# Kernel optimization log

Measured on AMD Instinct MI355X. Metric: run time of the kernel, lower is better.

The kernel has to match this reference:

```python
import jax, jax.numpy as jnp
import numpy as np

DIM = 4          # number of trunk networks (x, y, z, t)
H = 256          # hidden width for trunk and branch MLPs
R = 64           # CP rank
FD = 1           # field_dim
NF = 64          # Fourier feature half-width (B has shape (1, 64))
BRANCH_DIM = 256
DEPTH = 3        # MLP depth (3 hidden layers per eqx.nn.MLP semantics)


def _lin_init(key, out_dim, in_dim):
    return jax.random.normal(key, (out_dim, in_dim), dtype=jnp.float32) / jnp.sqrt(jnp.float32(in_dim))


def setup_inputs() -> dict:
    key = jax.random.key(0)
    ks = jax.random.split(key, 40)
    inp = {}
    # coordinate arrays, one per trunk: (N_i, 1)
    inp['x1'] = jax.random.uniform(ks[0], (64, 1), dtype=jnp.float32)
    inp['x2'] = jax.random.uniform(ks[1], (64, 1), dtype=jnp.float32)
    inp['x3'] = jax.random.uniform(ks[2], (64, 1), dtype=jnp.float32)
    inp['x4'] = jax.random.uniform(ks[3], (32, 1), dtype=jnp.float32)
    # branch input: batch of power maps, (B, branch_dim)
    inp['f'] = jax.random.normal(ks[4], (8, BRANCH_DIM), dtype=jnp.float32)
    # Fourier feature matrix B ~ 2*pi*N(0,1), shape (1, 64)
    inp['B'] = 2.0 * jnp.pi * jax.random.normal(ks[5], (1, NF), dtype=jnp.float32)
    # trunk ensemble params, stacked over the DIM trunks (all share shapes)
    inp['tW0'] = jnp.stack([_lin_init(ks[6 + i], H, 2 * NF) for i in range(DIM)])
    inp['tb0'] = jnp.zeros((DIM, H), dtype=jnp.float32)
    inp['tW1'] = jnp.stack([_lin_init(ks[10 + i], H, H) for i in range(DIM)])
    inp['tb1'] = jnp.zeros((DIM, H), dtype=jnp.float32)
    inp['tW2'] = jnp.stack([_lin_init(ks[14 + i], H, H) for i in range(DIM)])
    inp['tb2'] = jnp.zeros((DIM, H), dtype=jnp.float32)
    inp['tW3'] = jnp.stack([_lin_init(ks[18 + i], R * FD, H) for i in range(DIM)])
    inp['tb3'] = jnp.zeros((DIM, R * FD), dtype=jnp.float32)
    # branch MLP params
    inp['bW0'] = _lin_init(ks[30], H, BRANCH_DIM)
    inp['bb0'] = jnp.zeros((H,), dtype=jnp.float32)
    inp['bW1'] = _lin_init(ks[31], H, H)
    inp['bb1'] = jnp.zeros((H,), dtype=jnp.float32)
    inp['bW2'] = _lin_init(ks[32], H, H)
    inp['bb2'] = jnp.zeros((H,), dtype=jnp.float32)
    inp['bW3'] = _lin_init(ks[33], R * FD, H)
    inp['bb3'] = jnp.zeros((R * FD,), dtype=jnp.float32)
    return inp


def _forward(x1, x2, x3, x4, f, B,
             tW0, tb0, tW1, tb1, tW2, tb2, tW3, tb3,
             bW0, bb0, bW1, bb1, bW2, bb2, bW3, bb3):
    xs = [x1, x2, x3, x4]
    ts = []
    for i in range(DIM):
        p = xs[i] @ B                                  # (N_i, NF)
        feat = jnp.concatenate([jnp.cos(p), jnp.sin(p)], axis=1)  # (N_i, 2*NF)
        h = jax.nn.swish(feat @ tW0[i].T + tb0[i])
        h = jax.nn.swish(h @ tW1[i].T + tb1[i])
        h = jax.nn.swish(h @ tW2[i].T + tb2[i])
        t = (h @ tW3[i].T + tb3[i]).reshape(-1, FD, R)  # (N_i, y, z)
        ts.append(t)
    h = jax.nn.swish(f @ bW0.T + bb0)
    h = jax.nn.swish(h @ bW1.T + bb1)
    h = jax.nn.swish(h @ bW2.T + bb2)
    b = (h @ bW3.T + bb3).reshape(-1, FD, R)            # (B, y, z)
    # rank-R CP outer-product reconstruction: sum over z, shared field dim y
    return jnp.einsum('iyz,jyz,kyz,lyz,byz->bijkly',
                      ts[0], ts[1], ts[2], ts[3], b, optimize='optimal')


def reference(x1, x2, x3, x4, f, B,
              tW0, tb0, tW1, tb1, tW2, tb2, tW3, tb3,
              bW0, bb0, bW1, bb1, bW2, bb2, bW3, bb3):
    return _forward(x1, x2, x3, x4, f, B,
                    tW0, tb0, tW1, tb1, tW2, tb2, tW3, tb3,
                    bW0, bb0, bW1, bb1, bW2, bb2, bW3, bb3)
```

## Files before the change

### kernel.cpp

```cpp
#include <hip/hip_runtime.h>
#include <math.h>


#define HID 256
#define NFF 64

__global__ __launch_bounds__(256) void net_eval(
    const float* __restrict__ x1, const float* __restrict__ x2,
    const float* __restrict__ x3, const float* __restrict__ x4,
    const float* __restrict__ f,  const float* __restrict__ Bm,
    const float* __restrict__ tW0, const float* __restrict__ tb0,
    const float* __restrict__ tW1, const float* __restrict__ tb1,
    const float* __restrict__ tW2, const float* __restrict__ tb2,
    const float* __restrict__ tW3, const float* __restrict__ tb3,
    const float* __restrict__ bW0, const float* __restrict__ bb0,
    const float* __restrict__ bW1, const float* __restrict__ bb1,
    const float* __restrict__ bW2, const float* __restrict__ bb2,
    const float* __restrict__ bW3, const float* __restrict__ bb3,
    float* __restrict__ ws)
{
    __shared__ float bufA[HID];
    __shared__ float bufB[HID];
    const int t = threadIdx.x;
    const int bid = blockIdx.x;

    int net, row;
    if (bid < 192)      { net = bid >> 6; row = bid & 63; }
    else if (bid < 224) { net = 3;        row = bid - 192; }
    else                { net = 4;        row = bid - 224; }

    const float *W0, *B0v, *W1, *B1v, *W2, *B2v, *W3, *B3v;
    int in0;
    if (net < 4) {
        W0 = tW0 + (size_t)net * HID * 2 * NFF; B0v = tb0 + net * HID;
        W1 = tW1 + (size_t)net * HID * HID;     B1v = tb1 + net * HID;
        W2 = tW2 + (size_t)net * HID * HID;     B2v = tb2 + net * HID;
        W3 = tW3 + (size_t)net * 64 * HID;      B3v = tb3 + net * 64;
        in0 = 2 * NFF;
        const float* xp = (net == 0) ? x1 : (net == 1) ? x2 : (net == 2) ? x3 : x4;
        float xv = xp[row];
        if (t < 128) {
            float p = xv * Bm[t & 63];
            bufA[t] = (t < 64) ? cosf(p) : sinf(p);
        }
    } else {
        W0 = bW0; B0v = bb0; W1 = bW1; B1v = bb1;
        W2 = bW2; B2v = bb2; W3 = bW3; B3v = bb3;
        in0 = 256;
        bufA[t] = f[(size_t)row * 256 + t];
    }
    __syncthreads();

    {
        float acc = B0v[t];
        const float4* wr = (const float4*)(W0 + (size_t)t * in0);
        const float4* iv = (const float4*)bufA;
        const int n4 = in0 >> 2;
        for (int k = 0; k < n4; ++k) {
            float4 w = wr[k]; float4 v = iv[k];
            acc += w.x * v.x + w.y * v.y + w.z * v.z + w.w * v.w;
        }
        bufB[t] = acc / (1.0f + expf(-acc));
    }
    __syncthreads();

    {
        float acc = B1v[t];
        const float4* wr = (const float4*)(W1 + (size_t)t * HID);
        const float4* iv = (const float4*)bufB;
        for (int k = 0; k < HID / 4; ++k) {
            float4 w = wr[k]; float4 v = iv[k];
            acc += w.x * v.x + w.y * v.y + w.z * v.z + w.w * v.w;
        }
        bufA[t] = acc / (1.0f + expf(-acc));
    }
    __syncthreads();

    {
        float acc = B2v[t];
        const float4* wr = (const float4*)(W2 + (size_t)t * HID);
        const float4* iv = (const float4*)bufA;
        for (int k = 0; k < HID / 4; ++k) {
            float4 w = wr[k]; float4 v = iv[k];
            acc += w.x * v.x + w.y * v.y + w.z * v.z + w.w * v.w;
        }
        bufB[t] = acc / (1.0f + expf(-acc));
    }
    __syncthreads();

    if (t < 64) {
        float acc = B3v[t];
        const float4* wr = (const float4*)(W3 + (size_t)t * HID);
        const float4* iv = (const float4*)bufB;
        for (int k = 0; k < HID / 4; ++k) {
            float4 w = wr[k]; float4 v = iv[k];
            acc += w.x * v.x + w.y * v.y + w.z * v.z + w.w * v.w;
        }
        int base, stride;
        if      (net == 0) { base = 0;     stride = 64; }
        else if (net == 1) { base = 4096;  stride = 64; }
        else if (net == 2) { base = 8192;  stride = 64; }
        else if (net == 3) { base = 12288; stride = 32; }
        else               { base = 14336; stride = 8;  }
        ws[base + t * stride + row] = acc;
    }
}

__global__ __launch_bounds__(256) void cp_recon(
    const float* __restrict__ ws, float* __restrict__ out)
{
    __shared__ float t2s[64 * 64];
    __shared__ float t3s[64 * 32];
    __shared__ float sS[4 * 64];

    const int t = threadIdx.x;
    const int bid = blockIdx.x;
    const int b  = bid >> 10;
    const int i  = (bid >> 4) & 63;
    const int j0 = (bid & 15) * 4;

    #pragma unroll
    for (int m = 0; m < 16; ++m) {
        int g = t + m * 256;
        t2s[g] = ws[8192 + g];
    }
    #pragma unroll
    for (int m = 0; m < 8; ++m) {
        int g = t + m * 256;
        t3s[g] = ws[12288 + g];
    }
    {
        int jj = t >> 6;
        int z  = t & 63;
        sS[t] = ws[z * 64 + i] * ws[4096 + z * 64 + j0 + jj] * ws[14336 + z * 8 + b];
    }
    __syncthreads();

    const int jj   = t >> 6;
    const int lane = t & 63;
    const int k0   = (lane >> 3) * 8;
    const int l0   = (lane & 7) * 4;
    const float* sp = &sS[jj * 64];

    float4 acc[8];
    #pragma unroll
    for (int kk = 0; kk < 8; ++kk) acc[kk] = make_float4(0.f, 0.f, 0.f, 0.f);

    #pragma unroll 4
    for (int z = 0; z < 64; ++z) {
        float sz = sp[z];
        float4 t3v = *(const float4*)&t3s[z * 32 + l0];
        float4 a0  = *(const float4*)&t2s[z * 64 + k0];
        float4 a1  = *(const float4*)&t2s[z * 64 + k0 + 4];
        float4 u;
        u.x = sz * t3v.x; u.y = sz * t3v.y; u.z = sz * t3v.z; u.w = sz * t3v.w;
        float ks0 = a0.x, ks1 = a0.y, ks2 = a0.z, ks3 = a0.w;
        float ks4 = a1.x, ks5 = a1.y, ks6 = a1.z, ks7 = a1.w;
        acc[0].x += ks0 * u.x; acc[0].y += ks0 * u.y; acc[0].z += ks0 * u.z; acc[0].w += ks0 * u.w;
        acc[1].x += ks1 * u.x; acc[1].y += ks1 * u.y; acc[1].z += ks1 * u.z; acc[1].w += ks1 * u.w;
        acc[2].x += ks2 * u.x; acc[2].y += ks2 * u.y; acc[2].z += ks2 * u.z; acc[2].w += ks2 * u.w;
        acc[3].x += ks3 * u.x; acc[3].y += ks3 * u.y; acc[3].z += ks3 * u.z; acc[3].w += ks3 * u.w;
        acc[4].x += ks4 * u.x; acc[4].y += ks4 * u.y; acc[4].z += ks4 * u.z; acc[4].w += ks4 * u.w;
        acc[5].x += ks5 * u.x; acc[5].y += ks5 * u.y; acc[5].z += ks5 * u.z; acc[5].w += ks5 * u.w;
        acc[6].x += ks6 * u.x; acc[6].y += ks6 * u.y; acc[6].z += ks6 * u.z; acc[6].w += ks6 * u.w;
        acc[7].x += ks7 * u.x; acc[7].y += ks7 * u.y; acc[7].z += ks7 * u.z; acc[7].w += ks7 * u.w;
    }

    size_t base = ((size_t)((b * 64 + i) * 64 + (j0 + jj))) * 2048;
    float* op = out + base;
    #pragma unroll
    for (int kk = 0; kk < 8; ++kk) {
        *(float4*)&op[(k0 + kk) * 32 + l0] = acc[kk];
    }
}

extern "C" void kernel_launch(void* const* d_in, const int* in_sizes, int n_in,
                              void* d_out, int out_size, void* d_ws, size_t ws_size,
                              hipStream_t stream) {
    const float* x1  = (const float*)d_in[0];
    const float* x2  = (const float*)d_in[1];
    const float* x3  = (const float*)d_in[2];
    const float* x4  = (const float*)d_in[3];
    const float* f   = (const float*)d_in[4];
    const float* Bm  = (const float*)d_in[5];
    const float* tW0 = (const float*)d_in[6];
    const float* tb0 = (const float*)d_in[7];
    const float* tW1 = (const float*)d_in[8];
    const float* tb1 = (const float*)d_in[9];
    const float* tW2 = (const float*)d_in[10];
    const float* tb2 = (const float*)d_in[11];
    const float* tW3 = (const float*)d_in[12];
    const float* tb3 = (const float*)d_in[13];
    const float* bW0 = (const float*)d_in[14];
    const float* bb0 = (const float*)d_in[15];
    const float* bW1 = (const float*)d_in[16];
    const float* bb1 = (const float*)d_in[17];
    const float* bW2 = (const float*)d_in[18];
    const float* bb2 = (const float*)d_in[19];
    const float* bW3 = (const float*)d_in[20];
    const float* bb3 = (const float*)d_in[21];

    float* ws  = (float*)d_ws;
    float* out = (float*)d_out;

    hipLaunchKernelGGL(net_eval, dim3(232), dim3(256), 0, stream,
                       x1, x2, x3, x4, f, Bm,
                       tW0, tb0, tW1, tb1, tW2, tb2, tW3, tb3,
                       bW0, bb0, bW1, bb1, bW2, bb2, bW3, bb3, ws);
    hipLaunchKernelGGL(cp_recon, dim3(8192), dim3(256), 0, stream, ws, out);
}
```

Measured before the change: 399.9 us.

## Recast CP reconstruction as bf16 MFMA GEMM and warp-reduce MLP layers

```diff
diff --git a/kernel.cpp b/kernel.cpp
--- a/kernel.cpp
+++ b/kernel.cpp
@@ -2,8 +2,51 @@
 #include <math.h>
 
 
-#define HID 256
-#define NFF 64
+typedef float float4v __attribute__((ext_vector_type(4)));
+typedef short short8 __attribute__((ext_vector_type(8)));
+
+__device__ inline unsigned short f2bf(float f) {
+    union { float f; unsigned u; } c; c.f = f;
+    unsigned u = c.u;
+    unsigned r = (u + 0x7FFFu + ((u >> 16) & 1u)) >> 16;
+    return (unsigned short)r;
+}
+
+
+template<int IN, int OUT, bool ACT>
+__device__ inline void layer(const float* __restrict__ W,
+                             const float* __restrict__ Bv,
+                             const float* __restrict__ xin,
+                             float* __restrict__ yout,
+                             int t)
+{
+    const int lane = t & 63;
+    const int w    = t >> 6;
+    constexpr int C   = IN / 64;
+    constexpr int JPW = OUT / 4;
+
+    float xr[C];
+    #pragma unroll
+    for (int c = 0; c < C; ++c) xr[c] = xin[lane * C + c];
+
+    #pragma unroll 2
+    for (int jj = 0; jj < JPW; ++jj) {
+        int j = w * JPW + jj;
+        float s;
+        if (C == 4) {
+            float4 wv = ((const float4*)(W + (size_t)j * IN))[lane];
+            s = wv.x * xr[0] + wv.y * xr[1] + wv.z * xr[2] + wv.w * xr[3];
+        } else {
+            float2 wv = ((const float2*)(W + (size_t)j * IN))[lane];
+            s = wv.x * xr[0] + wv.y * xr[1];
+        }
+        #pragma unroll
+        for (int m = 32; m >= 1; m >>= 1) s += __shfl_xor(s, m, 64);
+        s += Bv[j];
+        if (ACT) s = s / (1.0f + expf(-s));
+        if (lane == 0) yout[j] = s;
+    }
+}
 
 __global__ __launch_bounds__(256) void net_eval(
     const float* __restrict__ x1, const float* __restrict__ x2,
@@ -19,9 +62,9 @@
     const float* __restrict__ bW3, const float* __restrict__ bb3,
     float* __restrict__ ws)
 {
-    __shared__ float bufA[HID];
-    __shared__ float bufB[HID];
-    const int t = threadIdx.x;
+    __shared__ float buf0[256];
+    __shared__ float buf1[256];
+    const int t   = threadIdx.x;
     const int bid = blockIdx.x;
 
     int net, row;
@@ -30,147 +73,131 @@
     else                { net = 4;        row = bid - 224; }
 
     const float *W0, *B0v, *W1, *B1v, *W2, *B2v, *W3, *B3v;
-    int in0;
     if (net < 4) {
-        W0 = tW0 + (size_t)net * HID * 2 * NFF; B0v = tb0 + net * HID;
-        W1 = tW1 + (size_t)net * HID * HID;     B1v = tb1 + net * HID;
-        W2 = tW2 + (size_t)net * HID * HID;     B2v = tb2 + net * HID;
-        W3 = tW3 + (size_t)net * 64 * HID;      B3v = tb3 + net * 64;
-        in0 = 2 * NFF;
+        W0 = tW0 + (size_t)net * 256 * 128; B0v = tb0 + net * 256;
+        W1 = tW1 + (size_t)net * 256 * 256; B1v = tb1 + net * 256;
+        W2 = tW2 + (size_t)net * 256 * 256; B2v = tb2 + net * 256;
+        W3 = tW3 + (size_t)net * 64 * 256;  B3v = tb3 + net * 64;
         const float* xp = (net == 0) ? x1 : (net == 1) ? x2 : (net == 2) ? x3 : x4;
         float xv = xp[row];
         if (t < 128) {
             float p = xv * Bm[t & 63];
-            bufA[t] = (t < 64) ? cosf(p) : sinf(p);
+            buf0[t] = (t < 64) ? cosf(p) : sinf(p);
         }
     } else {
         W0 = bW0; B0v = bb0; W1 = bW1; B1v = bb1;
         W2 = bW2; B2v = bb2; W3 = bW3; B3v = bb3;
-        in0 = 256;
-        bufA[t] = f[(size_t)row * 256 + t];
-    }
-    __syncthreads();
-
-    {
-        float acc = B0v[t];
-        const float4* wr = (const float4*)(W0 + (size_t)t * in0);
-        const float4* iv = (const float4*)bufA;
-        const int n4 = in0 >> 2;
-        for (int k = 0; k < n4; ++k) {
-            float4 w = wr[k]; float4 v = iv[k];
-            acc += w.x * v.x + w.y * v.y + w.z * v.z + w.w * v.w;
-        }
-        bufB[t] = acc / (1.0f + expf(-acc));
-    }
-    __syncthreads();
-
-    {
-        float acc = B1v[t];
-        const float4* wr = (const float4*)(W1 + (size_t)t * HID);
-        const float4* iv = (const float4*)bufB;
-        for (int k = 0; k < HID / 4; ++k) {
-            float4 w = wr[k]; float4 v = iv[k];
-            acc += w.x * v.x + w.y * v.y + w.z * v.z + w.w * v.w;
-        }
-        bufA[t] = acc / (1.0f + expf(-acc));
-    }
-    __syncthreads();
-
-    {
-        float acc = B2v[t];
-        const float4* wr = (const float4*)(W2 + (size_t)t * HID);
-        const float4* iv = (const float4*)bufA;
-        for (int k = 0; k < HID / 4; ++k) {
-            float4 w = wr[k]; float4 v = iv[k];
-            acc += w.x * v.x + w.y * v.y + w.z * v.z + w.w * v.w;
-        }
-        bufB[t] = acc / (1.0f + expf(-acc));
-    }
+        buf0[t] = f[(size_t)row * 256 + t];
+    }
+    __syncthreads();
+
+    if (net < 4) layer<128, 256, true>(W0, B0v, buf0, buf1, t);
+    else         layer<256, 256, true>(W0, B0v, buf0, buf1, t);
+    __syncthreads();
+    layer<256, 256, true>(W1, B1v, buf1, buf0, t);
+    __syncthreads();
+    layer<256, 256, true>(W2, B2v, buf0, buf1, t);
+    __syncthreads();
+    layer<256, 64, false>(W3, B3v, buf1, buf0, t);
     __syncthreads();
 
     if (t < 64) {
-        float acc = B3v[t];
-        const float4* wr = (const float4*)(W3 + (size_t)t * HID);
-        const float4* iv = (const float4*)bufB;
-        for (int k = 0; k < HID / 4; ++k) {
-            float4 w = wr[k]; float4 v = iv[k];
-            acc += w.x * v.x + w.y * v.y + w.z * v.z + w.w * v.w;
-        }
-        int base, stride;
-        if      (net == 0) { base = 0;     stride = 64; }
-        else if (net == 1) { base = 4096;  stride = 64; }
-        else if (net == 2) { base = 8192;  stride = 64; }
-        else if (net == 3) { base = 12288; stride = 32; }
-        else               { base = 14336; stride = 8;  }
-        ws[base + t * stride + row] = acc;
-    }
-}
-
-__global__ __launch_bounds__(256) void cp_recon(
+        int base;
+        if      (net == 0) base = 0;
+        else if (net == 1) base = 4096;
+        else if (net == 2) base = 8192;
+        else if (net == 3) base = 12288;
+        else               base = 14336;
+        ws[base + row * 64 + t] = buf0[t];
+    }
+}
+
+
+#define PAD 72
+
+__global__ __launch_bounds__(256) void cp_gemm(
     const float* __restrict__ ws, float* __restrict__ out)
 {
-    __shared__ float t2s[64 * 64];
-    __shared__ float t3s[64 * 32];
-    __shared__ float sS[4 * 64];
-
-    const int t = threadIdx.x;
-    const int bid = blockIdx.x;
-    const int b  = bid >> 10;
-    const int i  = (bid >> 4) & 63;
-    const int j0 = (bid & 15) * 4;
-
-    #pragma unroll
-    for (int m = 0; m < 16; ++m) {
-        int g = t + m * 256;
-        t2s[g] = ws[8192 + g];
-    }
-    #pragma unroll
-    for (int m = 0; m < 8; ++m) {
-        int g = t + m * 256;
-        t3s[g] = ws[12288 + g];
-    }
+    __shared__ __align__(16) unsigned short Ssh[128 * PAD];
+    __shared__ __align__(16) unsigned short Tsh[128 * PAD];
+
+    const int t    = threadIdx.x;
+    const int bid  = blockIdx.x;
+    const int mblk = bid >> 4;
+    const int nblk = bid & 15;
+    const int m0   = mblk * 128;
+    const int n0   = nblk * 128;
+
+    const float* t0p = ws;
+    const float* t1p = ws + 4096;
+    const float* t2p = ws + 8192;
+    const float* t3p = ws + 12288;
+    const float* brp = ws + 14336;
+
     {
-        int jj = t >> 6;
-        int z  = t & 63;
-        sS[t] = ws[z * 64 + i] * ws[4096 + z * 64 + j0 + jj] * ws[14336 + z * 8 + b];
-    }
-    __syncthreads();
-
-    const int jj   = t >> 6;
+        const int z     = t & 63;
+        const int rbase = t >> 6;
+        #pragma unroll
+        for (int it = 0; it < 32; ++it) {
+            int r = rbase + it * 4;
+            int m = m0 + r;
+            int b = m >> 12, i = (m >> 6) & 63, j = m & 63;
+            float v = t0p[i * 64 + z] * t1p[j * 64 + z] * brp[b * 64 + z];
+            Ssh[r * PAD + z] = f2bf(v);
+        }
+        #pragma unroll
+        for (int it = 0; it < 32; ++it) {
+            int nr = rbase + it * 4;
+            int n  = n0 + nr;
+            int k  = n >> 5, l = n & 31;
+            float v = t2p[k * 64 + z] * t3p[l * 64 + z];
+            Tsh[nr * PAD + z] = f2bf(v);
+        }
+    }
+    __syncthreads();
+
+    const int w    = t >> 6;
     const int lane = t & 63;
-    const int k0   = (lane >> 3) * 8;
-    const int l0   = (lane & 7) * 4;
-    const float* sp = &sS[jj * 64];
-
-    float4 acc[8];
-    #pragma unroll
-    for (int kk = 0; kk < 8; ++kk) acc[kk] = make_float4(0.f, 0.f, 0.f, 0.f);
-
-    #pragma unroll 4
-    for (int z = 0; z < 64; ++z) {
-        float sz = sp[z];
-        float4 t3v = *(const float4*)&t3s[z * 32 + l0];
-        float4 a0  = *(const float4*)&t2s[z * 64 + k0];
-        float4 a1  = *(const float4*)&t2s[z * 64 + k0 + 4];
-        float4 u;
-        u.x = sz * t3v.x; u.y = sz * t3v.y; u.z = sz * t3v.z; u.w = sz * t3v.w;
-        float ks0 = a0.x, ks1 = a0.y, ks2 = a0.z, ks3 = a0.w;
-        float ks4 = a1.x, ks5 = a1.y, ks6 = a1.z, ks7 = a1.w;
-        acc[0].x += ks0 * u.x; acc[0].y += ks0 * u.y; acc[0].z += ks0 * u.z; acc[0].w += ks0 * u.w;
-        acc[1].x += ks1 * u.x; acc[1].y += ks1 * u.y; acc[1].z += ks1 * u.z; acc[1].w += ks1 * u.w;
-        acc[2].x += ks2 * u.x; acc[2].y += ks2 * u.y; acc[2].z += ks2 * u.z; acc[2].w += ks2 * u.w;
-        acc[3].x += ks3 * u.x; acc[3].y += ks3 * u.y; acc[3].z += ks3 * u.z; acc[3].w += ks3 * u.w;
-        acc[4].x += ks4 * u.x; acc[4].y += ks4 * u.y; acc[4].z += ks4 * u.z; acc[4].w += ks4 * u.w;
-        acc[5].x += ks5 * u.x; acc[5].y += ks5 * u.y; acc[5].z += ks5 * u.z; acc[5].w += ks5 * u.w;
-        acc[6].x += ks6 * u.x; acc[6].y += ks6 * u.y; acc[6].z += ks6 * u.z; acc[6].w += ks6 * u.w;
-        acc[7].x += ks7 * u.x; acc[7].y += ks7 * u.y; acc[7].z += ks7 * u.z; acc[7].w += ks7 * u.w;
-    }
-
-    size_t base = ((size_t)((b * 64 + i) * 64 + (j0 + jj))) * 2048;
-    float* op = out + base;
-    #pragma unroll
-    for (int kk = 0; kk < 8; ++kk) {
-        *(float4*)&op[(k0 + kk) * 32 + l0] = acc[kk];
+    const int wm   = w >> 1;
+    const int wn   = w & 1;
+    const int l16  = lane & 15;
+    const int quad = lane >> 4;
+
+    float4v acc[4][4];
+    #pragma unroll
+    for (int mt = 0; mt < 4; ++mt)
+        #pragma unroll
+        for (int nt = 0; nt < 4; ++nt)
+            acc[mt][nt] = (float4v){0.f, 0.f, 0.f, 0.f};
+
+    #pragma unroll
+    for (int ks = 0; ks < 2; ++ks) {
+        short8 a[4], b[4];
+        #pragma unroll
+        for (int mt = 0; mt < 4; ++mt)
+            a[mt] = *(const short8*)&Ssh[(wm * 64 + mt * 16 + l16) * PAD + ks * 32 + quad * 8];
+        #pragma unroll
+        for (int nt = 0; nt < 4; ++nt)
+            b[nt] = *(const short8*)&Tsh[(wn * 64 + nt * 16 + l16) * PAD + ks * 32 + quad * 8];
+        #pragma unroll
+        for (int mt = 0; mt < 4; ++mt)
+            #pragma unroll
+            for (int nt = 0; nt < 4; ++nt)
+                acc[mt][nt] = __builtin_amdgcn_mfma_f32_16x16x32_bf16(
+                    a[mt], b[nt], acc[mt][nt], 0, 0, 0);
+    }
+
+    #pragma unroll
+    for (int mt = 0; mt < 4; ++mt) {
+        int mrow = m0 + wm * 64 + mt * 16 + quad * 4;
+        #pragma unroll
+        for (int nt = 0; nt < 4; ++nt) {
+            int ncol = n0 + wn * 64 + nt * 16 + l16;
+            float* op = out + (size_t)mrow * 2048 + ncol;
+            #pragma unroll
+            for (int r = 0; r < 4; ++r)
+                op[(size_t)r * 2048] = acc[mt][nt][r];
+        }
     }
 }
 
@@ -207,5 +234,5 @@
                        x1, x2, x3, x4, f, Bm,
                        tW0, tb0, tW1, tb1, tW2, tb2, tW3, tb3,
                        bW0, bb0, bW1, bb1, bW2, bb2, bW3, bb3, ws);
-    hipLaunchKernelGGL(cp_recon, dim3(8192), dim3(256), 0, stream, ws, out);
-}
+    hipLaunchKernelGGL(cp_gemm, dim3(4096), dim3(256), 0, stream, ws, out);
+}
```

Measured after the change: 472.4 us. 18.1% more time.
